# Kernel tuning notes

Hardware: AMD Instinct MI355X
Metric: run time of the kernel (lower is better)

Reference implementation:

```python
import jax, jax.numpy as jnp
import numpy as np

DIM = 128
N_HEADS = 16
HEAD_DIM = DIM // N_HEADS  # 8
HIDDEN = 344  # multiple_of=8 rounding of int(2*4*128/3)
B, S = 4, 2048


def setup_inputs() -> dict:
    key = jax.random.key(0)
    ks = jax.random.split(key, 8)
    sc = 0.05
    return {
        "x": jax.random.normal(ks[0], (B, S, DIM), dtype=jnp.float32),
        "wq": jax.random.normal(ks[1], (DIM, DIM), dtype=jnp.float32) * sc,
        "wk": jax.random.normal(ks[2], (DIM, DIM), dtype=jnp.float32) * sc,
        "wv": jax.random.normal(ks[3], (DIM, DIM), dtype=jnp.float32) * sc,
        "wo": jax.random.normal(ks[4], (DIM, DIM), dtype=jnp.float32) * sc,
        "w1": jax.random.normal(ks[5], (DIM, HIDDEN), dtype=jnp.float32) * sc,
        "w3": jax.random.normal(ks[6], (DIM, HIDDEN), dtype=jnp.float32) * sc,
        "w2": jax.random.normal(ks[7], (HIDDEN, DIM), dtype=jnp.float32) * sc,
    }


def reference(x, wq, wk, wv, wo, w1, w3, w2):
    bsz, seqlen, _ = x.shape
    # --- Attention (no scaling, no mask, per source) ---
    q = (x @ wq).reshape(bsz, seqlen, N_HEADS, HEAD_DIM)
    k = (x @ wk).reshape(bsz, seqlen, N_HEADS, HEAD_DIM)
    v = (x @ wv).reshape(bsz, seqlen, N_HEADS, HEAD_DIM)
    # scores: [B, H, S, S]
    scores = jnp.einsum("bqhd,bkhd->bhqk", q, k)
    probs = jax.nn.softmax(scores.astype(jnp.float32), axis=-1).astype(q.dtype)
    attn = jnp.einsum("bhqk,bkhd->bqhd", probs, v).reshape(bsz, seqlen, DIM)
    h = x + attn @ wo
    # --- SwiGLU FFN ---
    ffn = (jax.nn.silu(h @ w1) * (h @ w3)) @ w2
    return h + ffn
```

## Files before the change

kernel.cpp:

```cpp
#include <hip/hip_runtime.h>
#include <hip/hip_bf16.h>
#include <stdint.h>
#include <math.h>

typedef __attribute__((ext_vector_type(8))) short short8;
typedef __attribute__((ext_vector_type(4))) float f32x4;

#define NTHREADS 256
#define DIM 128
#define NH 16
#define HD 8
#define HIDDEN 344
#define HIDP 352
#define BATCH 4
#define SEQ 2048
#define MROWS (BATCH * SEQ)
#define LOG2E 1.4426950408889634f

static __device__ __forceinline__ uint16_t f2bf(float f) {
  union { float f; uint32_t u; } v; v.f = f;
  uint32_t r = v.u + 0x7FFFu + ((v.u >> 16) & 1u);
  return (uint16_t)(r >> 16);
}
static __device__ __forceinline__ uint32_t pk2(float lo, float hi) {
  union { __hip_bfloat162 b; uint32_t u; } c;
  c.b = __float22bfloat162_rn(make_float2(lo, hi));
  return c.u;
}
#define MAGIC_BF 12599163.0f
static __device__ __forceinline__ uint32_t pke2(float a, float b) {
  const float ua = fmaf(a, 128.0f, MAGIC_BF);
  const float ub = fmaf(b, 128.0f, MAGIC_BF);
  return __builtin_amdgcn_perm(__builtin_bit_cast(uint32_t, ub),
                               __builtin_bit_cast(uint32_t, ua), 0x05040100u);
}
static __device__ __forceinline__ f32x4 mfma32(short8 a, short8 b, f32x4 c) {
  return __builtin_amdgcn_mfma_f32_16x16x32_bf16(a, b, c, 0, 0, 0);
}

__global__ __launch_bounds__(256) void prep_kernel(
    const float* __restrict__ wq,
    const float* __restrict__ wk, const float* __restrict__ wv,
    const float* __restrict__ wo, const float* __restrict__ w1,
    const float* __restrict__ w3, const float* __restrict__ w2,
    uint16_t* __restrict__ qkv_t,
    uint16_t* __restrict__ wo_t,  uint16_t* __restrict__ w1_t,
    uint16_t* __restrict__ w3_t,  uint16_t* __restrict__ w2_t)
{
  const int nt  = gridDim.x * blockDim.x;
  const int tid = blockIdx.x * blockDim.x + threadIdx.x;
  for (int i = tid; i < 384 * 128; i += nt) {
    int n = i >> 7, k = i & 127;
    const float* w = (n < 128) ? wq : ((n < 256) ? wk : wv);
    const float s = (n < 128) ? LOG2E : 1.0f;
    qkv_t[i] = f2bf(w[k * 128 + (n & 127)] * s);
  }
  for (int i = tid; i < 128 * 128; i += nt) {
    int n = i >> 7, k = i & 127;
    wo_t[i] = f2bf(wo[k * 128 + n]);
  }
  for (int i = tid; i < 384 * 128; i += nt) {
    int n = i >> 7, k = i & 127;
    w1_t[i] = (n < HIDDEN) ? f2bf(w1[k * HIDDEN + n]) : (uint16_t)0;
    w3_t[i] = (n < HIDDEN) ? f2bf(w3[k * HIDDEN + n]) : (uint16_t)0;
  }
  for (int i = tid; i < 128 * HIDP; i += nt) {
    int n = i / HIDP, k = i - n * HIDP;
    w2_t[i] = (k < HIDDEN) ? f2bf(w2[k * 128 + n]) : (uint16_t)0;
  }
}

__global__ __launch_bounds__(256, 4) void qkv_gemm(
    const float* __restrict__ Av, const uint16_t* __restrict__ B1t,
    uint16_t* __restrict__ outb,
    uint16_t* __restrict__ kc_o, uint16_t* __restrict__ vt_o)
{
  const int tid = threadIdx.x;
  const int w = tid >> 6, l = tid & 63;
  const int lg = l >> 4, lm = l & 15;
  const int row0 = blockIdx.x * 64 + w * 16;
  const int col0 = blockIdx.y * 64;

  const uint16_t* Bp = B1t + (size_t)(col0 + lm) * 128 + lg * 8;
  short8 bA0 = *(const short8*)(Bp);
  short8 bA1 = *(const short8*)(Bp + 32);
  short8 bA2 = *(const short8*)(Bp + 64);
  short8 bA3 = *(const short8*)(Bp + 96);

  short8 af[4];
  const float* Af = Av + (size_t)(row0 + lm) * 128 + lg * 8;
#pragma unroll
  for (int ks = 0; ks < 4; ++ks) {
    const f32x4 a0 = *(const f32x4*)(Af + ks * 32);
    const f32x4 a1 = *(const f32x4*)(Af + ks * 32 + 4);
    union { uint32_t u[4]; short8 s8; } cv;
    cv.u[0] = pk2(a0[0], a0[1]); cv.u[1] = pk2(a0[2], a0[3]);
    cv.u[2] = pk2(a1[0], a1[1]); cv.u[3] = pk2(a1[2], a1[3]);
    af[ks] = cv.s8;
  }

  f32x4 acc[4];
#pragma unroll
  for (int t = 0; t < 4; ++t) acc[t] = (f32x4){0.f, 0.f, 0.f, 0.f};

  short8 bB0 = *(const short8*)(Bp + 2048);
  short8 bB1 = *(const short8*)(Bp + 2048 + 32);
  short8 bB2 = *(const short8*)(Bp + 2048 + 64);
  short8 bB3 = *(const short8*)(Bp + 2048 + 96);
  acc[0] = mfma32(af[0], bA0, acc[0]);
  acc[0] = mfma32(af[1], bA1, acc[0]);
  acc[0] = mfma32(af[2], bA2, acc[0]);
  acc[0] = mfma32(af[3], bA3, acc[0]);
  bA0 = *(const short8*)(Bp + 4096);
  bA1 = *(const short8*)(Bp + 4096 + 32);
  bA2 = *(const short8*)(Bp + 4096 + 64);
  bA3 = *(const short8*)(Bp + 4096 + 96);
  acc[1] = mfma32(af[0], bB0, acc[1]);
  acc[1] = mfma32(af[1], bB1, acc[1]);
  acc[1] = mfma32(af[2], bB2, acc[1]);
  acc[1] = mfma32(af[3], bB3, acc[1]);
  bB0 = *(const short8*)(Bp + 6144);
  bB1 = *(const short8*)(Bp + 6144 + 32);
  bB2 = *(const short8*)(Bp + 6144 + 64);
  bB3 = *(const short8*)(Bp + 6144 + 96);
  acc[2] = mfma32(af[0], bA0, acc[2]);
  acc[2] = mfma32(af[1], bA1, acc[2]);
  acc[2] = mfma32(af[2], bA2, acc[2]);
  acc[2] = mfma32(af[3], bA3, acc[2]);
  acc[3] = mfma32(af[0], bB0, acc[3]);
  acc[3] = mfma32(af[1], bB1, acc[3]);
  acc[3] = mfma32(af[2], bB2, acc[3]);
  acc[3] = mfma32(af[3], bB3, acc[3]);

#pragma unroll
  for (int t = 0; t < 4; ++t) {
#pragma unroll
    for (int r = 0; r < 4; ++r) {
      const int row = row0 + lg * 4 + r;
      const int col = col0 + t * 16 + lm;
      const float v = acc[t][r];
      const int bb = row >> 11, ss = row & 2047;
      if (col < 128) {
        outb[(size_t)row * 128 + col] = f2bf(v);
      } else if (col < 256) {
        const int c = col - 128;
        kc_o[((size_t)((bb << 4) + (c >> 3)) * SEQ + ss) * 8 + (c & 7)] = f2bf(v);
      } else {
        const int c = col - 256;
        vt_o[((size_t)(bb * 128 + c)) * SEQ + ss] = f2bf(v);
      }
    }
  }
}

__global__ __launch_bounds__(256, 4) void attn_kernel(
    const uint16_t* __restrict__ qb,
    const uint16_t* __restrict__ kc,
    const uint16_t* __restrict__ vt,
    uint16_t* __restrict__ attn_o)
{
  __shared__ __attribute__((aligned(16))) float part[4][64][16];

  const int tid = threadIdx.x;
  const int w = tid >> 6, l = tid & 63;
  const int lg = l >> 4, lm = l & 15;
  int bid = blockIdx.x;
  bid = (bid & 7) * 256 + (bid >> 3);
  const int qc = bid & 31;
  const int bh = bid >> 5;
  const int b = bh >> 4, h = bh & 15;
  const int q0 = qc * 64;
  const int kh = w;

  const short8 zero8 = {0, 0, 0, 0, 0, 0, 0, 0};
  const f32x4 zero4 = {0.f, 0.f, 0.f, 0.f};
  const short ob = (short)0x3F80;
  const short8 ones8 = {ob, ob, ob, ob, ob, ob, ob, ob};

  short8 qf0 = zero8, qf1 = zero8, qf2 = zero8, qf3 = zero8;
  if (lg == 0) {
    const uint16_t* qp = qb + (size_t)(b * SEQ + q0 + lm) * DIM + h * HD;
    qf0 = *(const short8*)(qp);
    qf1 = *(const short8*)(qp + 16 * DIM);
    qf2 = *(const short8*)(qp + 32 * DIM);
    qf3 = *(const short8*)(qp + 48 * DIM);
  }

  const uint16_t* kp = kc + (size_t)bh * SEQ * HD +
                       (kh * 512 + 8 * (lm >> 2) + (lm & 3)) * HD;
  const uint16_t* vp = vt + (size_t)(bh * HD + (lm & 7)) * SEQ + kh * 512 + lg * 8;

  short8 k0 = zero8, k1 = zero8, k2 = zero8, k3 = zero8;
  short8 v0 = (lm == 8) ? ones8 : zero8;
  short8 v1 = v0;

  f32x4 acc0 = zero4, acc1 = zero4, acc2 = zero4, acc3 = zero4;

#define LK()                                       \
  do { if (lg == 0) {                              \
    k0 = *(const short8*)(kp);                     \
    k1 = *(const short8*)(kp + 32);                \
    k2 = *(const short8*)(kp + 256);               \
    k3 = *(const short8*)(kp + 288); }             \
    kp += 512; } while (0)

#define LV()                                       \
  do { if (lm < HD) {                              \
    v0 = *(const short8*)(vp);                     \
    v1 = *(const short8*)(vp + 32); }              \
    vp += 64; } while (0)

#define PACKP(SA, SB, OUT)                 \
  do { union { uint32_t u[4]; short8 s; } _t; \
    _t.u[0] = pke2(SA[0], SA[1]);          \
    _t.u[1] = pke2(SA[2], SA[3]);          \
    _t.u[2] = pke2(SB[0], SB[1]);          \
    _t.u[3] = pke2(SB[2], SB[3]);          \
    OUT = _t.s; } while (0)

  LK();
  LV();

#pragma unroll 1
  for (int it = 0; it < 8; ++it) {
    short8 p0, p1;
    f32x4 sa0 = mfma32(k0, qf0, zero4);
    f32x4 sa1 = mfma32(k1, qf0, zero4);
    f32x4 sa2 = mfma32(k2, qf0, zero4);
    f32x4 sa3 = mfma32(k3, qf0, zero4);
    f32x4 sb0 = mfma32(k0, qf1, zero4);
    f32x4 sb1 = mfma32(k1, qf1, zero4);
    f32x4 sb2 = mfma32(k2, qf1, zero4);
    f32x4 sb3 = mfma32(k3, qf1, zero4);
    PACKP(sa0, sa1, p0);
    PACKP(sa2, sa3, p1);
    acc0 = mfma32(v0, p0, acc0);
    acc0 = mfma32(v1, p1, acc0);
    sa0 = mfma32(k0, qf2, zero4);
    sa1 = mfma32(k1, qf2, zero4);
    sa2 = mfma32(k2, qf2, zero4);
    sa3 = mfma32(k3, qf2, zero4);
    PACKP(sb0, sb1, p0);
    PACKP(sb2, sb3, p1);
    acc1 = mfma32(v0, p0, acc1);
    acc1 = mfma32(v1, p1, acc1);
    sb0 = mfma32(k0, qf3, zero4);
    sb1 = mfma32(k1, qf3, zero4);
    sb2 = mfma32(k2, qf3, zero4);
    sb3 = mfma32(k3, qf3, zero4);
    LK();
    PACKP(sa0, sa1, p0);
    PACKP(sa2, sa3, p1);
    acc2 = mfma32(v0, p0, acc2);
    acc2 = mfma32(v1, p1, acc2);
    PACKP(sb0, sb1, p0);
    PACKP(sb2, sb3, p1);
    acc3 = mfma32(v0, p0, acc3);
    acc3 = mfma32(v1, p1, acc3);
    LV();
  }

#undef LK
#undef LV
#undef PACKP

  *(f32x4*)&part[w][l][0]  = acc0;
  *(f32x4*)&part[w][l][4]  = acc1;
  *(f32x4*)&part[w][l][8]  = acc2;
  *(f32x4*)&part[w][l][12] = acc3;
  __syncthreads();

  {
    const f32x4 m = (*(const f32x4*)&part[0][l][w * 4] +
                     *(const f32x4*)&part[1][l][w * 4]) +
                    (*(const f32x4*)&part[2][l][w * 4] +
                     *(const f32x4*)&part[3][l][w * 4]);
    const float inv = 1.0f / __shfl(m[0], 32 + lm);
    if (lg < 2) {
      const size_t o = (size_t)(b * SEQ + q0 + w * 16 + lm) * DIM + h * HD + lg * 4;
      *(uint32_t*)(attn_o + o)     = pk2(m[0] * inv, m[1] * inv);
      *(uint32_t*)(attn_o + o + 2) = pk2(m[2] * inv, m[3] * inv);
    }
  }
}

__global__ __launch_bounds__(512, 4) void ffn_kernel(
    const uint16_t* __restrict__ attn_o,
    const float* __restrict__ x,
    const uint16_t* __restrict__ wo_t,
    const uint16_t* __restrict__ w1_t,
    const uint16_t* __restrict__ w3_t,
    const uint16_t* __restrict__ w2_t,
    float* __restrict__ out)
{
  __shared__ __attribute__((aligned(16))) uint16_t h_l[16][136];
  __shared__ __attribute__((aligned(16))) uint16_t u_l[16][360];

  const int tid = threadIdx.x;
  const int w = tid >> 6, l = tid & 63;
  const int lg = l >> 4, lm = l & 15;
  const int R0 = blockIdx.x * 16;

  short8 af[4], wof[4], b1a[4], b3a[4];
  {
    const uint16_t* Ap = attn_o + (size_t)(R0 + lm) * 128 + lg * 8;
    const uint16_t* Bp = wo_t + (size_t)(w * 16 + lm) * 128 + lg * 8;
    const uint16_t* B1p = w1_t + (size_t)(w * 16 + lm) * 128 + lg * 8;
    const uint16_t* B3p = w3_t + (size_t)(w * 16 + lm) * 128 + lg * 8;
#pragma unroll
    for (int ks = 0; ks < 4; ++ks) {
      af[ks]  = *(const short8*)(Ap + ks * 32);
      wof[ks] = *(const short8*)(Bp + ks * 32);
      b1a[ks] = *(const short8*)(B1p + ks * 32);
      b3a[ks] = *(const short8*)(B3p + ks * 32);
    }
  }

  float hreg[4];
  {
    f32x4 acc = (f32x4){0.f, 0.f, 0.f, 0.f};
#pragma unroll
    for (int ks = 0; ks < 4; ++ks)
      acc = mfma32(af[ks], wof[ks], acc);
#pragma unroll
    for (int r = 0; r < 4; ++r) {
      const float h = acc[r] + x[(size_t)(R0 + lg * 4 + r) * 128 + w * 16 + lm];
      hreg[r] = h;
      h_l[lg * 4 + r][w * 16 + lm] = f2bf(h);
    }
  }
  __syncthreads();

  short8 af2[4];
#pragma unroll
  for (int ks = 0; ks < 4; ++ks)
    af2[ks] = *(const short8*)&h_l[lm][ks * 32 + lg * 8];

  {
    f32x4 ag = (f32x4){0.f, 0.f, 0.f, 0.f};
    f32x4 ae = (f32x4){0.f, 0.f, 0.f, 0.f};
#pragma unroll
    for (int ks = 0; ks < 4; ++ks) {
      ag = mfma32(af2[ks], b1a[ks], ag);
      ae = mfma32(af2[ks], b3a[ks], ae);
    }
    const int ct2 = w + 8;
    const uint16_t* B1p = w1_t + (size_t)(ct2 * 16 + lm) * 128 + lg * 8;
    const uint16_t* B3p = w3_t + (size_t)(ct2 * 16 + lm) * 128 + lg * 8;
#pragma unroll
    for (int ks = 0; ks < 4; ++ks) {
      b1a[ks] = *(const short8*)(B1p + ks * 32);
      b3a[ks] = *(const short8*)(B3p + ks * 32);
    }
#pragma unroll
    for (int r = 0; r < 4; ++r) {
      const float g = ag[r];
      const float u = g / (1.f + __expf(-g)) * ae[r];
      u_l[lg * 4 + r][w * 16 + lm] = f2bf(u);
    }
  }
  {
    const int ct = w + 8;
    f32x4 ag = (f32x4){0.f, 0.f, 0.f, 0.f};
    f32x4 ae = (f32x4){0.f, 0.f, 0.f, 0.f};
#pragma unroll
    for (int ks = 0; ks < 4; ++ks) {
      ag = mfma32(af2[ks], b1a[ks], ag);
      ae = mfma32(af2[ks], b3a[ks], ae);
    }
    if (w < 6) {
      const int ct3 = w + 16;
      const uint16_t* B1p = w1_t + (size_t)(ct3 * 16 + lm) * 128 + lg * 8;
      const uint16_t* B3p = w3_t + (size_t)(ct3 * 16 + lm) * 128 + lg * 8;
#pragma unroll
      for (int ks = 0; ks < 4; ++ks) {
        b1a[ks] = *(const short8*)(B1p + ks * 32);
        b3a[ks] = *(const short8*)(B3p + ks * 32);
      }
    }
#pragma unroll
    for (int r = 0; r < 4; ++r) {
      const float g = ag[r];
      const float u = g / (1.f + __expf(-g)) * ae[r];
      u_l[lg * 4 + r][ct * 16 + lm] = f2bf(u);
    }
  }
  if (w < 6) {
    const int ct = w + 16;
    f32x4 ag = (f32x4){0.f, 0.f, 0.f, 0.f};
    f32x4 ae = (f32x4){0.f, 0.f, 0.f, 0.f};
#pragma unroll
    for (int ks = 0; ks < 4; ++ks) {
      ag = mfma32(af2[ks], b1a[ks], ag);
      ae = mfma32(af2[ks], b3a[ks], ae);
    }
#pragma unroll
    for (int r = 0; r < 4; ++r) {
      const float g = ag[r];
      const float u = g / (1.f + __expf(-g)) * ae[r];
      u_l[lg * 4 + r][ct * 16 + lm] = f2bf(u);
    }
  }
  __syncthreads();

  {
    short8 w2f0, w2f1, w2f2, w2f3;
    const uint16_t* Bp = w2_t + (size_t)(w * 16 + lm) * HIDP + lg * 8;
    w2f0 = *(const short8*)(Bp);
    w2f1 = *(const short8*)(Bp + 32);
    w2f2 = *(const short8*)(Bp + 64);
    w2f3 = *(const short8*)(Bp + 96);
    f32x4 acc = (f32x4){0.f, 0.f, 0.f, 0.f};
    acc = mfma32(*(const short8*)&u_l[lm][0 * 32 + lg * 8], w2f0, acc);
    w2f0 = *(const short8*)(Bp + 128);
    acc = mfma32(*(const short8*)&u_l[lm][1 * 32 + lg * 8], w2f1, acc);
    w2f1 = *(const short8*)(Bp + 160);
    acc = mfma32(*(const short8*)&u_l[lm][2 * 32 + lg * 8], w2f2, acc);
    w2f2 = *(const short8*)(Bp + 192);
    acc = mfma32(*(const short8*)&u_l[lm][3 * 32 + lg * 8], w2f3, acc);
    w2f3 = *(const short8*)(Bp + 224);
    acc = mfma32(*(const short8*)&u_l[lm][4 * 32 + lg * 8], w2f0, acc);
    w2f0 = *(const short8*)(Bp + 256);
    acc = mfma32(*(const short8*)&u_l[lm][5 * 32 + lg * 8], w2f1, acc);
    w2f1 = *(const short8*)(Bp + 288);
    acc = mfma32(*(const short8*)&u_l[lm][6 * 32 + lg * 8], w2f2, acc);
    w2f2 = *(const short8*)(Bp + 320);
    acc = mfma32(*(const short8*)&u_l[lm][7 * 32 + lg * 8], w2f3, acc);
    acc = mfma32(*(const short8*)&u_l[lm][8 * 32 + lg * 8], w2f0, acc);
    acc = mfma32(*(const short8*)&u_l[lm][9 * 32 + lg * 8], w2f1, acc);
    acc = mfma32(*(const short8*)&u_l[lm][10 * 32 + lg * 8], w2f2, acc);
#pragma unroll
    for (int r = 0; r < 4; ++r)
      out[(size_t)(R0 + lg * 4 + r) * 128 + w * 16 + lm] = hreg[r] + acc[r];
  }
}

extern "C" void kernel_launch(void* const* d_in, const int* in_sizes, int n_in,
                              void* d_out, int out_size, void* d_ws, size_t ws_size,
                              hipStream_t stream) {
  const float* x  = (const float*)d_in[0];
  const float* wq = (const float*)d_in[1];
  const float* wk = (const float*)d_in[2];
  const float* wv = (const float*)d_in[3];
  const float* wo = (const float*)d_in[4];
  const float* w1 = (const float*)d_in[5];
  const float* w3 = (const float*)d_in[6];
  const float* w2 = (const float*)d_in[7];
  float* out = (float*)d_out;

  char* ws = (char*)d_ws;
  size_t off = 0;
  auto alloc = [&](size_t bytes) {
    size_t o = off;
    off += (bytes + 255) & ~(size_t)255;
    return o;
  };
  uint16_t* qkv_t  = (uint16_t*)(ws + alloc(384 * 128 * 2));
  uint16_t* wo_t   = (uint16_t*)(ws + alloc(128 * 128 * 2));
  uint16_t* w1_t   = (uint16_t*)(ws + alloc(384 * 128 * 2));
  uint16_t* w3_t   = (uint16_t*)(ws + alloc(384 * 128 * 2));
  uint16_t* w2_t   = (uint16_t*)(ws + alloc(128 * HIDP * 2));
  uint16_t* q_buf  = (uint16_t*)(ws + alloc((size_t)MROWS * DIM * 2));
  uint16_t* kc_b   = (uint16_t*)(ws + alloc((size_t)MROWS * DIM * 2));
  uint16_t* vt_b   = (uint16_t*)(ws + alloc((size_t)MROWS * DIM * 2));
  uint16_t* attn_o = (uint16_t*)(ws + alloc((size_t)MROWS * DIM * 2));

  prep_kernel<<<512, 256, 0, stream>>>(wq, wk, wv, wo, w1, w3, w2,
                                       qkv_t, wo_t, w1_t, w3_t, w2_t);
  qkv_gemm<<<dim3(MROWS / 64, 6), 256, 0, stream>>>(
      x, qkv_t, q_buf, kc_b, vt_b);
  attn_kernel<<<dim3(BATCH * NH * (SEQ / 64)), 256, 0, stream>>>(
      q_buf, kc_b, vt_b, attn_o);
  ffn_kernel<<<dim3(MROWS / 16), 512, 0, stream>>>(
      attn_o, x, wo_t, w1_t, w3_t, w2_t, out);
}
```

Baseline: 64.54 us.

## Double attention query tile per block and split FFN MFMA accumulator chains

The attention kernel now processes 128 queries per block instead of 64, so each loaded K/V fragment is reused across eight query tiles and the grid halves. The shared partial-sum buffer doubles, and each wave reduces and writes two query tiles. Separately, the Wo and W2 MFMA chains in the FFN kernel are split into two independent accumulators to shorten dependency chains. The larger per-thread state (eight Q fragments and eight accumulators) raises register pressure and halves the number of blocks, which may reduce occupancy and latency hiding.

```diff
diff --git a/kernel.cpp b/kernel.cpp
--- a/kernel.cpp
+++ b/kernel.cpp
@@ -159,17 +159,17 @@
     const uint16_t* __restrict__ vt,
     uint16_t* __restrict__ attn_o)
 {
-  __shared__ __attribute__((aligned(16))) float part[4][64][16];
+  __shared__ __attribute__((aligned(16))) float part[4][64][32];
 
   const int tid = threadIdx.x;
   const int w = tid >> 6, l = tid & 63;
   const int lg = l >> 4, lm = l & 15;
   int bid = blockIdx.x;
-  bid = (bid & 7) * 256 + (bid >> 3);
-  const int qc = bid & 31;
-  const int bh = bid >> 5;
+  bid = (bid & 7) * 128 + (bid >> 3);
+  const int qc = bid & 15;
+  const int bh = bid >> 4;
   const int b = bh >> 4, h = bh & 15;
-  const int q0 = qc * 64;
+  const int q0 = qc * 128;
   const int kh = w;
 
   const short8 zero8 = {0, 0, 0, 0, 0, 0, 0, 0};
@@ -177,13 +177,12 @@
   const short ob = (short)0x3F80;
   const short8 ones8 = {ob, ob, ob, ob, ob, ob, ob, ob};
 
-  short8 qf0 = zero8, qf1 = zero8, qf2 = zero8, qf3 = zero8;
-  if (lg == 0) {
-    const uint16_t* qp = qb + (size_t)(b * SEQ + q0 + lm) * DIM + h * HD;
-    qf0 = *(const short8*)(qp);
-    qf1 = *(const short8*)(qp + 16 * DIM);
-    qf2 = *(const short8*)(qp + 32 * DIM);
-    qf3 = *(const short8*)(qp + 48 * DIM);
+  short8 qf[8];
+#pragma unroll
+  for (int t = 0; t < 8; ++t) {
+    qf[t] = zero8;
+    if (lg == 0)
+      qf[t] = *(const short8*)(qb + (size_t)(b * SEQ + q0 + t * 16 + lm) * DIM + h * HD);
   }
 
   const uint16_t* kp = kc + (size_t)bh * SEQ * HD +
@@ -194,7 +193,9 @@
   short8 v0 = (lm == 8) ? ones8 : zero8;
   short8 v1 = v0;
 
-  f32x4 acc0 = zero4, acc1 = zero4, acc2 = zero4, acc3 = zero4;
+  f32x4 acc[8];
+#pragma unroll
+  for (int t = 0; t < 8; ++t) acc[t] = zero4;
 
 #define LK()                                       \
   do { if (lg == 0) {                              \
@@ -223,61 +224,40 @@
 
 #pragma unroll 1
   for (int it = 0; it < 8; ++it) {
-    short8 p0, p1;
-    f32x4 sa0 = mfma32(k0, qf0, zero4);
-    f32x4 sa1 = mfma32(k1, qf0, zero4);
-    f32x4 sa2 = mfma32(k2, qf0, zero4);
-    f32x4 sa3 = mfma32(k3, qf0, zero4);
-    f32x4 sb0 = mfma32(k0, qf1, zero4);
-    f32x4 sb1 = mfma32(k1, qf1, zero4);
-    f32x4 sb2 = mfma32(k2, qf1, zero4);
-    f32x4 sb3 = mfma32(k3, qf1, zero4);
-    PACKP(sa0, sa1, p0);
-    PACKP(sa2, sa3, p1);
-    acc0 = mfma32(v0, p0, acc0);
-    acc0 = mfma32(v1, p1, acc0);
-    sa0 = mfma32(k0, qf2, zero4);
-    sa1 = mfma32(k1, qf2, zero4);
-    sa2 = mfma32(k2, qf2, zero4);
-    sa3 = mfma32(k3, qf2, zero4);
-    PACKP(sb0, sb1, p0);
-    PACKP(sb2, sb3, p1);
-    acc1 = mfma32(v0, p0, acc1);
-    acc1 = mfma32(v1, p1, acc1);
-    sb0 = mfma32(k0, qf3, zero4);
-    sb1 = mfma32(k1, qf3, zero4);
-    sb2 = mfma32(k2, qf3, zero4);
-    sb3 = mfma32(k3, qf3, zero4);
-    LK();
-    PACKP(sa0, sa1, p0);
-    PACKP(sa2, sa3, p1);
-    acc2 = mfma32(v0, p0, acc2);
-    acc2 = mfma32(v1, p1, acc2);
-    PACKP(sb0, sb1, p0);
-    PACKP(sb2, sb3, p1);
-    acc3 = mfma32(v0, p0, acc3);
-    acc3 = mfma32(v1, p1, acc3);
-    LV();
+#pragma unroll
+    for (int t = 0; t < 8; ++t) {
+      f32x4 s0 = mfma32(k0, qf[t], zero4);
+      f32x4 s1 = mfma32(k1, qf[t], zero4);
+      f32x4 s2 = mfma32(k2, qf[t], zero4);
+      f32x4 s3 = mfma32(k3, qf[t], zero4);
+      if (t == 7) LK();
+      short8 p0, p1;
+      PACKP(s0, s1, p0);
+      PACKP(s2, s3, p1);
+      acc[t] = mfma32(v0, p0, acc[t]);
+      acc[t] = mfma32(v1, p1, acc[t]);
+      if (t == 7) LV();
+    }
   }
 
 #undef LK
 #undef LV
 #undef PACKP
 
-  *(f32x4*)&part[w][l][0]  = acc0;
-  *(f32x4*)&part[w][l][4]  = acc1;
-  *(f32x4*)&part[w][l][8]  = acc2;
-  *(f32x4*)&part[w][l][12] = acc3;
+#pragma unroll
+  for (int t = 0; t < 8; ++t) *(f32x4*)&part[w][l][t * 4] = acc[t];
   __syncthreads();
 
-  {
-    const f32x4 m = (*(const f32x4*)&part[0][l][w * 4] +
-                     *(const f32x4*)&part[1][l][w * 4]) +
-                    (*(const f32x4*)&part[2][l][w * 4] +
-                     *(const f32x4*)&part[3][l][w * 4]);
+#pragma unroll
+  for (int j = 0; j < 2; ++j) {
+    const int tt = w * 2 + j;
+    const f32x4 m = (*(const f32x4*)&part[0][l][tt * 4] +
+                     *(const f32x4*)&part[1][l][tt * 4]) +
+                    (*(const f32x4*)&part[2][l][tt * 4] +
+                     *(const f32x4*)&part[3][l][tt * 4]);
     const float inv = 1.0f / __shfl(m[0], 32 + lm);
     if (lg < 2) {
-      const size_t o = (size_t)(b * SEQ + q0 + w * 16 + lm) * DIM + h * HD + lg * 4;
+      const size_t o = (size_t)(b * SEQ + q0 + tt * 16 + lm) * DIM + h * HD + lg * 4;
       *(uint32_t*)(attn_o + o)     = pk2(m[0] * inv, m[1] * inv);
       *(uint32_t*)(attn_o + o + 2) = pk2(m[2] * inv, m[3] * inv);
     }
@@ -318,10 +298,13 @@
 
   float hreg[4];
   {
-    f32x4 acc = (f32x4){0.f, 0.f, 0.f, 0.f};
-#pragma unroll
-    for (int ks = 0; ks < 4; ++ks)
-      acc = mfma32(af[ks], wof[ks], acc);
+    f32x4 a0 = (f32x4){0.f, 0.f, 0.f, 0.f};
+    f32x4 a1 = (f32x4){0.f, 0.f, 0.f, 0.f};
+    a0 = mfma32(af[0], wof[0], a0);
+    a1 = mfma32(af[1], wof[1], a1);
+    a0 = mfma32(af[2], wof[2], a0);
+    a1 = mfma32(af[3], wof[3], a1);
+    const f32x4 acc = a0 + a1;
 #pragma unroll
     for (int r = 0; r < 4; ++r) {
       const float h = acc[r] + x[(size_t)(R0 + lg * 4 + r) * 128 + w * 16 + lm];
@@ -410,25 +393,27 @@
     w2f1 = *(const short8*)(Bp + 32);
     w2f2 = *(const short8*)(Bp + 64);
     w2f3 = *(const short8*)(Bp + 96);
-    f32x4 acc = (f32x4){0.f, 0.f, 0.f, 0.f};
-    acc = mfma32(*(const short8*)&u_l[lm][0 * 32 + lg * 8], w2f0, acc);
+    f32x4 acce = (f32x4){0.f, 0.f, 0.f, 0.f};
+    f32x4 acco = (f32x4){0.f, 0.f, 0.f, 0.f};
+    acce = mfma32(*(const short8*)&u_l[lm][0 * 32 + lg * 8], w2f0, acce);
     w2f0 = *(const short8*)(Bp + 128);
-    acc = mfma32(*(const short8*)&u_l[lm][1 * 32 + lg * 8], w2f1, acc);
+    acco = mfma32(*(const short8*)&u_l[lm][1 * 32 + lg * 8], w2f1, acco);
     w2f1 = *(const short8*)(Bp + 160);
-    acc = mfma32(*(const short8*)&u_l[lm][2 * 32 + lg * 8], w2f2, acc);
+    acce = mfma32(*(const short8*)&u_l[lm][2 * 32 + lg * 8], w2f2, acce);
     w2f2 = *(const short8*)(Bp + 192);
-    acc = mfma32(*(const short8*)&u_l[lm][3 * 32 + lg * 8], w2f3, acc);
+    acco = mfma32(*(const short8*)&u_l[lm][3 * 32 + lg * 8], w2f3, acco);
     w2f3 = *(const short8*)(Bp + 224);
-    acc = mfma32(*(const short8*)&u_l[lm][4 * 32 + lg * 8], w2f0, acc);
+    acce = mfma32(*(const short8*)&u_l[lm][4 * 32 + lg * 8], w2f0, acce);
     w2f0 = *(const short8*)(Bp + 256);
-    acc = mfma32(*(const short8*)&u_l[lm][5 * 32 + lg * 8], w2f1, acc);
+    acco = mfma32(*(const short8*)&u_l[lm][5 * 32 + lg * 8], w2f1, acco);
     w2f1 = *(const short8*)(Bp + 288);
-    acc = mfma32(*(const short8*)&u_l[lm][6 * 32 + lg * 8], w2f2, acc);
+    acce = mfma32(*(const short8*)&u_l[lm][6 * 32 + lg * 8], w2f2, acce);
     w2f2 = *(const short8*)(Bp + 320);
-    acc = mfma32(*(const short8*)&u_l[lm][7 * 32 + lg * 8], w2f3, acc);
-    acc = mfma32(*(const short8*)&u_l[lm][8 * 32 + lg * 8], w2f0, acc);
-    acc = mfma32(*(const short8*)&u_l[lm][9 * 32 + lg * 8], w2f1, acc);
-    acc = mfma32(*(const short8*)&u_l[lm][10 * 32 + lg * 8], w2f2, acc);
+    acco = mfma32(*(const short8*)&u_l[lm][7 * 32 + lg * 8], w2f3, acco);
+    acce = mfma32(*(const short8*)&u_l[lm][8 * 32 + lg * 8], w2f0, acce);
+    acco = mfma32(*(const short8*)&u_l[lm][9 * 32 + lg * 8], w2f1, acco);
+    acce = mfma32(*(const short8*)&u_l[lm][10 * 32 + lg * 8], w2f2, acce);
+    const f32x4 acc = acce + acco;
 #pragma unroll
     for (int r = 0; r < 4; ++r)
       out[(size_t)(R0 + lg * 4 + r) * 128 + w * 16 + lm] = hreg[r] + acc[r];
@@ -469,7 +454,7 @@
                                        qkv_t, wo_t, w1_t, w3_t, w2_t);
   qkv_gemm<<<dim3(MROWS / 64, 6), 256, 0, stream>>>(
       x, qkv_t, q_buf, kc_b, vt_b);
-  attn_kernel<<<dim3(BATCH * NH * (SEQ / 64)), 256, 0, stream>>>(
+  attn_kernel<<<dim3(BATCH * NH * (SEQ / 128)), 256, 0, stream>>>(
       q_buf, kc_b, vt_b, attn_o);
   ffn_kernel<<<dim3(MROWS / 16), 512, 0, stream>>>(
       attn_o, x, wo_t, w1_t, w3_t, w2_t, out);
```

New measurement: 63.52 us. About the same (-1.6%).
